# Optimization experiments

Hardware: AMD Instinct MI355X
Metric: run time of the kernel (lower is better)

The kernel has to match this reference:

```python
import jax, jax.numpy as jnp
import numpy as np

PATCH = 16
HIDDEN = 1024
NUM_HEADS = 16
HEAD_DIM = HIDDEN // NUM_HEADS


def sinusoidal_pe(n, d):
    # standard transformer sinusoidal positional encoding, shape [n, d]
    pos = np.arange(n, dtype=np.float32)[:, None]
    i = np.arange(0, d, 2, dtype=np.float32)[None, :]
    ang = pos / np.power(10000.0, i / d)
    pe = np.zeros((n, d), dtype=np.float32)
    pe[:, 0::2] = np.sin(ang)
    pe[:, 1::2] = np.cos(ang)
    return jnp.asarray(pe)


def patch_embed(x, w, b):
    # Conv2d(kernel=stride=PATCH) == non-overlapping patch GEMM
    B, C, H, W = x.shape
    hp, wp = H // PATCH, W // PATCH
    xp = x.reshape(B, C, hp, PATCH, wp, PATCH)
    t = jnp.einsum('bchpwq,dcpq->bhwd', xp, w)  # [B, hp, wp, D]
    return t.reshape(B, hp * wp, -1) + b        # [B, N, D]


def _fit(x, w, b):
    t = patch_embed(x, w, b)
    t = t + sinusoidal_pe(t.shape[1], t.shape[2])
    B, N, _ = t.shape
    return t.reshape(B, N, NUM_HEADS, HEAD_DIM).transpose(0, 2, 1, 3)  # [B,H,N,hd]


def setup_inputs() -> dict:
    key = jax.random.key(0)
    ks = jax.random.split(key, 9)
    B, C, H, W = 16, 3, 512, 512
    return {
        'q_img': jax.random.normal(ks[0], (B, C, H, W), jnp.float32),
        'k_img': jax.random.normal(ks[1], (B, C, H, W), jnp.float32),
        'v_img': jax.random.normal(ks[2], (B, C, H, W), jnp.float32),
        'wq': jax.random.normal(ks[3], (HIDDEN, C, PATCH, PATCH), jnp.float32) * 0.02,
        'bq': jax.random.normal(ks[4], (HIDDEN,), jnp.float32) * 0.02,
        'wk': jax.random.normal(ks[5], (HIDDEN, C, PATCH, PATCH), jnp.float32) * 0.02,
        'bk': jax.random.normal(ks[6], (HIDDEN,), jnp.float32) * 0.02,
        'wv': jax.random.normal(ks[7], (HIDDEN, C, PATCH, PATCH), jnp.float32) * 0.02,
        'bv': jax.random.normal(ks[8], (HIDDEN,), jnp.float32) * 0.02,
    }


def reference(q_img, k_img, v_img, wq, bq, wk, bk, wv, bv):
    q = _fit(q_img, wq, bq)  # [B,H,N,hd]
    k = _fit(k_img, wk, bk)
    v = _fit(v_img, wv, bv)
    q = jax.nn.softmax(q, axis=-1)   # softmax over head_dim
    k = jax.nn.softmax(k, axis=-2)   # softmax over tokens
    scores = jnp.einsum('bhnd,bhne->bhde', k, v)   # k^T v : [B,H,hd,hd]
    ctx = jnp.einsum('bhnd,bhde->bhne', q, scores)  # [B,H,N,hd]
    B, h, N, hd = ctx.shape
    return ctx.transpose(0, 2, 1, 3).reshape(B, N, h * hd)  # [B,N,hidden]
```

## Files before the change

kernel.cpp:

```cpp
#include <hip/hip_runtime.h>
#include <hip/hip_bf16.h>


typedef float  f32x4  __attribute__((ext_vector_type(4)));
typedef __bf16 bf16x8 __attribute__((ext_vector_type(8)));
typedef __bf16 bf16x4 __attribute__((ext_vector_type(4)));

#define LN10000 9.210340371976184f

__device__ __forceinline__ unsigned short f2bf_bits(float f){
  union { float f; unsigned u; } a; a.f = f;
  unsigned r = a.u + 0x7FFFu + ((a.u >> 16) & 1u);
  return (unsigned short)(r >> 16);
}

__device__ __forceinline__ void gload16(const void* g, void* l){
  __builtin_amdgcn_global_load_lds((__attribute__((address_space(1))) void*)g,
                                   (__attribute__((address_space(3))) void*)l,
                                   16, 0, 0);
}


__global__ __launch_bounds__(256) void k_prep_w(
    const float* __restrict__ wq, const float* __restrict__ wk,
    const float* __restrict__ wv, unsigned short* __restrict__ wbf)
{
  int i = blockIdx.x*256 + threadIdx.x;
  if (i >= 589824) return;
  int z = i / 196608;
  int r = i - z*196608;
  const float* src = (z==0) ? wq : (z==1 ? wk : wv);
  f32x4 v = ((const f32x4*)src)[r];
  unsigned lo = (unsigned)f2bf_bits(v[0]) | ((unsigned)f2bf_bits(v[1]) << 16);
  unsigned hh = (unsigned)f2bf_bits(v[2]) | ((unsigned)f2bf_bits(v[3]) << 16);
  ((uint2*)wbf)[i] = make_uint2(lo, hh);
}

__global__ __launch_bounds__(256) void k_prep_pe(float* __restrict__ pe)
{
  int i = blockIdx.x*256 + threadIdx.x;
  if (i >= 1048576) return;
  int n = i >> 10, dd = i & 1023;
  float ex  = (float)(dd & ~1) * (1.0f/1024.0f);
  float ang = (float)n * expf(-LN10000 * ex);
  pe[i] = (dd & 1) ? cosf(ang) : sinf(ang);
}

__global__ __launch_bounds__(256) void k_prep_x(
    const float* __restrict__ xq, const float* __restrict__ xk,
    const float* __restrict__ xv, unsigned short* __restrict__ x_bf)
{
  int i = blockIdx.x*256 + threadIdx.x;
  if (i >= 4718592) return;
  int z = i / 1572864;
  int r = i - z*1572864;
  const float* src = (z==0) ? xq : (z==1 ? xk : xv);
  f32x4 a = ((const f32x4*)src)[r*2];
  f32x4 b = ((const f32x4*)src)[r*2+1];
  uint4 o;
  o.x = (unsigned)f2bf_bits(a[0]) | ((unsigned)f2bf_bits(a[1]) << 16);
  o.y = (unsigned)f2bf_bits(a[2]) | ((unsigned)f2bf_bits(a[3]) << 16);
  o.z = (unsigned)f2bf_bits(b[0]) | ((unsigned)f2bf_bits(b[1]) << 16);
  o.w = (unsigned)f2bf_bits(b[2]) | ((unsigned)f2bf_bits(b[3]) << 16);
  ((uint4*)x_bf)[i] = o;
}


__global__ __launch_bounds__(256, 2) void k_embed(
    const unsigned short* __restrict__ x_bf,
    const unsigned short* __restrict__ wbf,
    const float* __restrict__ bq, const float* __restrict__ bk,
    const float* __restrict__ bv, const float* __restrict__ pe,
    unsigned short* __restrict__ t_bf)
{
  __shared__ __align__(16) unsigned short ldsA[2][128*64];
  __shared__ __align__(16) unsigned short ldsB[2][128*64];

  const int tid = threadIdx.x;
  int flat = blockIdx.x + (blockIdx.y << 3) + (blockIdx.z << 10);
  int orig = (flat & 7)*384 + (flat >> 3);
  const int z   = orig >> 10;
  const int rem = orig & 1023;
  const int m0  = (rem >> 3) * 128;
  const int d0  = (rem & 7) * 128;

  const unsigned short* xbz = x_bf + (size_t)z*12582912u;
  const unsigned short* wz  = wbf + z*786432;
  const float* bias = (z==0) ? bq : (z==1 ? bk : bv);
  unsigned short* tout = t_bf + (size_t)z*16777216u;

  int aRowG[4], aKK[4];
#pragma unroll
  for (int i=0;i<4;i++){
    int L   = i*4096 + tid*16;
    int row = L >> 7;
    int U   = L ^ ((row & 7) << 4);
    aKK[i]  = (U & 127) >> 1;
    int m   = m0 + row;
    int bimg = m >> 10, nt = m & 1023;
    aRowG[i] = bimg*786432 + (nt>>5)*8192 + (nt&31)*16;
  }
  int bOff[4];
#pragma unroll
  for (int i=0;i<4;i++){
    int L   = i*4096 + tid*16;
    int row = L >> 7;
    int U   = L ^ ((row & 7) << 4);
    bOff[i] = (d0 + row)*768 + ((U >> 1) & 63);
  }

  const int lane = tid & 63;
  const int wid  = tid >> 6;
  const int ln   = lane & 15, hi4 = lane >> 4;
  const int wm   = wid >> 1,  wn  = wid & 1;

  f32x4 acc[4][4] = {};

#define STAGE(BUF, KS) do{                                                  \
    _Pragma("unroll")                                                       \
    for (int i=0;i<4;i++){                                                  \
      int k  = (KS)*64 + aKK[i];                                            \
      int c  = k >> 8, r2 = k & 255;                                        \
      gload16(xbz + aRowG[i] + c*262144 + (r2>>4)*512 + (r2 & 15),          \
              (char*)(&ldsA[BUF][0]) + i*4096 + wid*1024);                  \
    }                                                                       \
    _Pragma("unroll")                                                       \
    for (int i=0;i<4;i++){                                                  \
      gload16(wz + bOff[i] + (KS)*64,                                       \
              (char*)(&ldsB[BUF][0]) + i*4096 + wid*1024);                  \
    } }while(0)

  STAGE(0, 0);
  for (int ks=0; ks<12; ++ks){
    int cur = ks & 1;
    if (ks < 11){
      STAGE(cur^1, ks+1);
      asm volatile("s_waitcnt vmcnt(8)" ::: "memory");
    } else {
      asm volatile("s_waitcnt vmcnt(0)" ::: "memory");
    }
    __builtin_amdgcn_sched_barrier(0);
    __builtin_amdgcn_s_barrier();
    __builtin_amdgcn_sched_barrier(0);

    const char* pA = (const char*)&ldsA[cur][0];
    const char* pB = (const char*)&ldsB[cur][0];
#pragma unroll
    for (int kc=0; kc<2; ++kc){
      bf16x8 af[4], bfr[4];
#pragma unroll
      for (int mi=0;mi<4;mi++){
        int row  = wm*64 + mi*16 + ln;
        int byte = (row*128 + kc*64 + hi4*16) ^ ((row & 7) << 4);
        af[mi] = *(const bf16x8*)(pA + byte);
      }
#pragma unroll
      for (int ni=0;ni<4;ni++){
        int row  = wn*64 + ni*16 + ln;
        int byte = (row*128 + kc*64 + hi4*16) ^ ((row & 7) << 4);
        bfr[ni] = *(const bf16x8*)(pB + byte);
      }
#pragma unroll
      for (int mi=0;mi<4;mi++)
#pragma unroll
        for (int ni=0;ni<4;ni++)
          acc[mi][ni] = __builtin_amdgcn_mfma_f32_16x16x32_bf16(
              af[mi], bfr[ni], acc[mi][ni], 0, 0, 0);
    }

    __builtin_amdgcn_sched_barrier(0);
    __builtin_amdgcn_s_barrier();
  }
#undef STAGE

  float bias4[4];
#pragma unroll
  for (int ni=0;ni<4;ni++) bias4[ni] = bias[d0 + wn*64 + ni*16 + ln];

#pragma unroll
  for (int mi=0;mi<4;mi++){
#pragma unroll
    for (int r=0;r<4;r++){
      int m    = m0 + wm*64 + mi*16 + hi4*4 + r;
      int ntok = m & 1023;
      float vv[4];
#pragma unroll
      for (int ni=0;ni<4;ni++){
        int dd = d0 + wn*64 + ni*16 + ln;
        vv[ni] = acc[mi][ni][r] + bias4[ni] + pe[ntok*1024 + dd];
      }
      size_t base = (size_t)m*1024 + d0 + wn*64 + ln;
      if (z == 0){
        float ex0=__expf(vv[0]), ex1=__expf(vv[1]),
              ex2=__expf(vv[2]), ex3=__expf(vv[3]);
        float ps = ex0+ex1+ex2+ex3;
        ps += __shfl_xor(ps, 1); ps += __shfl_xor(ps, 2);
        ps += __shfl_xor(ps, 4); ps += __shfl_xor(ps, 8);
        float w = 1.0f / ps;
        tout[base +  0] = f2bf_bits(ex0*w);  tout[base + 16] = f2bf_bits(ex1*w);
        tout[base + 32] = f2bf_bits(ex2*w);  tout[base + 48] = f2bf_bits(ex3*w);
      } else if (z == 1){
        tout[base +  0] = f2bf_bits(__expf(vv[0]));
        tout[base + 16] = f2bf_bits(__expf(vv[1]));
        tout[base + 32] = f2bf_bits(__expf(vv[2]));
        tout[base + 48] = f2bf_bits(__expf(vv[3]));
      } else {
        tout[base +  0] = f2bf_bits(vv[0]); tout[base + 16] = f2bf_bits(vv[1]);
        tout[base + 32] = f2bf_bits(vv[2]); tout[base + 48] = f2bf_bits(vv[3]);
      }
    }
  }
}


__global__ __launch_bounds__(512) void k_scores(
    const __bf16* __restrict__ t_bf, float* __restrict__ scoresOut)
{
  __shared__ __align__(16) float lds[4][4096];
  __shared__ float ksumLds[8][64];

  const int tid = threadIdx.x;
  const int bh  = blockIdx.x;
  const int b   = bh >> 4, h = bh & 15;
  const __bf16* kbase = t_bf + 16777216u + (size_t)b*1048576u + h*64;
  const __bf16* vbase = t_bf + 33554432u + (size_t)b*1048576u + h*64;

  const int dq = tid & 15, eg = (tid>>4) & 3, npart = tid >> 6;
  const int srow = tid >> 3;
  const int dcol = (tid & 7) * 8;

#define STAGE(BUF, CH) do{                                                \
    size_t g = (size_t)((CH)*64 + srow)*1024 + dcol;                      \
    bf16x8 k8 = *(const bf16x8*)(kbase + g);                              \
    bf16x8 v8 = *(const bf16x8*)(vbase + g);                              \
    f32x4 e0, e1, w0, w1;                                                 \
    e0[0]=(float)k8[0]; e0[1]=(float)k8[1]; e0[2]=(float)k8[2]; e0[3]=(float)k8[3]; \
    e1[0]=(float)k8[4]; e1[1]=(float)k8[5]; e1[2]=(float)k8[6]; e1[3]=(float)k8[7]; \
    w0[0]=(float)v8[0]; w0[1]=(float)v8[1]; w0[2]=(float)v8[2]; w0[3]=(float)v8[3]; \
    w1[0]=(float)v8[4]; w1[1]=(float)v8[5]; w1[2]=(float)v8[6]; w1[3]=(float)v8[7]; \
    *(f32x4*)(&lds[BUF][srow*64 + dcol])       = e0;                      \
    *(f32x4*)(&lds[BUF][srow*64 + dcol + 4])   = e1;                      \
    *(f32x4*)(&lds[2+(BUF)][srow*64 + dcol])     = w0;                    \
    *(f32x4*)(&lds[2+(BUF)][srow*64 + dcol + 4]) = w1;                    \
  }while(0)

  float acc[4][16] = {};
  float kp[4] = {0.f,0.f,0.f,0.f};

  STAGE(0, 0);
  __syncthreads();
  for (int ch=0; ch<16; ++ch){
    int cur = ch & 1;
    if (ch < 15) STAGE(cur^1, ch+1);
    for (int nn = npart; nn < 64; nn += 8){
      f32x4 ek4 = *(const f32x4*)(&lds[cur][nn*64 + dq*4]);
      f32x4 v0  = *(const f32x4*)(&lds[2+cur][nn*64 + eg*16 + 0]);
      f32x4 v1  = *(const f32x4*)(&lds[2+cur][nn*64 + eg*16 + 4]);
      f32x4 v2  = *(const f32x4*)(&lds[2+cur][nn*64 + eg*16 + 8]);
      f32x4 v3  = *(const f32x4*)(&lds[2+cur][nn*64 + eg*16 + 12]);
#pragma unroll
      for (int i2=0;i2<4;i2++){
        kp[i2] += ek4[i2];
#pragma unroll
        for (int j=0;j<4;j++){
          acc[i2][j+0]  += ek4[i2]*v0[j];
          acc[i2][j+4]  += ek4[i2]*v1[j];
          acc[i2][j+8]  += ek4[i2]*v2[j];
          acc[i2][j+12] += ek4[i2]*v3[j];
        }
      }
    }
    __syncthreads();
  }
#undef STAGE

  if (eg == 0){
#pragma unroll
    for (int i2=0;i2<4;i2++) ksumLds[npart][dq*4 + i2] = kp[i2];
  }

  if (npart < 4){
    float* pb = &lds[npart][0];
#pragma unroll
    for (int i2=0;i2<4;i2++){
      int base = (dq*4 + i2)*64 + eg*16;
      f32x4 a0; a0[0]=acc[i2][0];  a0[1]=acc[i2][1];  a0[2]=acc[i2][2];  a0[3]=acc[i2][3];
      f32x4 a1; a1[0]=acc[i2][4];  a1[1]=acc[i2][5];  a1[2]=acc[i2][6];  a1[3]=acc[i2][7];
      f32x4 a2; a2[0]=acc[i2][8];  a2[1]=acc[i2][9];  a2[2]=acc[i2][10]; a2[3]=acc[i2][11];
      f32x4 a3; a3[0]=acc[i2][12]; a3[1]=acc[i2][13]; a3[2]=acc[i2][14]; a3[3]=acc[i2][15];
      *(f32x4*)(pb + base + 0)  = a0;
      *(f32x4*)(pb + base + 4)  = a1;
      *(f32x4*)(pb + base + 8)  = a2;
      *(f32x4*)(pb + base + 12) = a3;
    }
  }
  __syncthreads();
  if (npart >= 4){
    float* pb = &lds[npart-4][0];
#pragma unroll
    for (int i2=0;i2<4;i2++){
      int base = (dq*4 + i2)*64 + eg*16;
#pragma unroll
      for (int q=0;q<4;q++){
        f32x4 cu = *(const f32x4*)(pb + base + 4*q);
        cu[0]+=acc[i2][4*q+0]; cu[1]+=acc[i2][4*q+1];
        cu[2]+=acc[i2][4*q+2]; cu[3]+=acc[i2][4*q+3];
        *(f32x4*)(pb + base + 4*q) = cu;
      }
    }
  }
  __syncthreads();

  float* outp = scoresOut + (size_t)bh*4096;
#pragma unroll
  for (int i=0;i<2;i++){
    int idx = tid + 512*i;
    int q4  = idx*4;
    int d   = idx >> 4;
    float rk = 1.0f / (ksumLds[0][d]+ksumLds[1][d]+ksumLds[2][d]+ksumLds[3][d]
                      +ksumLds[4][d]+ksumLds[5][d]+ksumLds[6][d]+ksumLds[7][d]);
    f32x4 s = *(const f32x4*)(&lds[0][q4]) + *(const f32x4*)(&lds[1][q4])
            + *(const f32x4*)(&lds[2][q4]) + *(const f32x4*)(&lds[3][q4]);
    s[0]*=rk; s[1]*=rk; s[2]*=rk; s[3]*=rk;
    *(f32x4*)(outp + q4) = s;
  }
}


__global__ __launch_bounds__(256) void k_ctx(
    const __bf16* __restrict__ t_bf, const float* __restrict__ scoresIn,
    float* __restrict__ out)
{
  __shared__ __align__(16) float S[64*64];
  __shared__ __align__(16) float qnT[64*132];

  const int tid   = threadIdx.x;
  const int bh    = blockIdx.y;
  const int b     = bh >> 4, h = bh & 15;
  const int chunk = blockIdx.x;
  const __bf16* qbase = t_bf + (size_t)b*1048576u + h*64;

#pragma unroll
  for (int i=0;i<4;i++){
    int q4 = (tid + 256*i)*4;
    *(f32x4*)(S + q4) = *(const f32x4*)(scoresIn + (size_t)bh*4096 + q4);
  }

  const int lane = tid & 63, w = tid >> 6;
  const int pos = lane & 15, rq = lane >> 4;
#pragma unroll
  for (int p=0;p<8;p++){
    int nl = w*32 + p*4 + rq;
    int n  = chunk*128 + nl;
    bf16x4 qv = *(const bf16x4*)(qbase + (size_t)n*1024 + pos*4);
    qnT[(pos*4+0)*132 + nl] = (float)qv[0];
    qnT[(pos*4+1)*132 + nl] = (float)qv[1];
    qnT[(pos*4+2)*132 + nl] = (float)qv[2];
    qnT[(pos*4+3)*132 + nl] = (float)qv[3];
  }
  __syncthreads();

  const int eq = tid & 15, tg = tid >> 4;
  float acc[8][4] = {};
  for (int d=0; d<64; ++d){
    f32x4 s4 = *(const f32x4*)(S   + d*64  + eq*4);
    f32x4 q0 = *(const f32x4*)(qnT + d*132 + tg*8 + 0);
    f32x4 q1 = *(const f32x4*)(qnT + d*132 + tg*8 + 4);
#pragma unroll
    for (int j=0;j<4;j++){
      acc[0][j] += q0[0]*s4[j];
      acc[1][j] += q0[1]*s4[j];
      acc[2][j] += q0[2]*s4[j];
      acc[3][j] += q0[3]*s4[j];
      acc[4][j] += q1[0]*s4[j];
      acc[5][j] += q1[1]*s4[j];
      acc[6][j] += q1[2]*s4[j];
      acc[7][j] += q1[3]*s4[j];
    }
  }
#pragma unroll
  for (int i2=0;i2<8;i2++){
    int n = chunk*128 + tg*8 + i2;
    f32x4 o; o[0]=acc[i2][0]; o[1]=acc[i2][1]; o[2]=acc[i2][2]; o[3]=acc[i2][3];
    *(f32x4*)(out + (size_t)(b*1024 + n)*1024 + h*64 + eq*4) = o;
  }
}


extern "C" void kernel_launch(void* const* d_in, const int* in_sizes, int n_in,
                              void* d_out, int out_size, void* d_ws, size_t ws_size,
                              hipStream_t stream)
{
  const float* q_img = (const float*)d_in[0];
  const float* k_img = (const float*)d_in[1];
  const float* v_img = (const float*)d_in[2];
  const float* wq    = (const float*)d_in[3];
  const float* bq    = (const float*)d_in[4];
  const float* wk    = (const float*)d_in[5];
  const float* bk    = (const float*)d_in[6];
  const float* wv    = (const float*)d_in[7];
  const float* bv    = (const float*)d_in[8];
  float* out = (float*)d_out;
  char*  ws  = (char*)d_ws;

  unsigned short* t_bf   = (unsigned short*)ws;
  unsigned short* wbf    = (unsigned short*)(ws + 0x6000000);
  float*          pe     = (float*)(ws + 0x6480000);
  float*          scores = (float*)(ws + 0x6880000);
  unsigned short* x_bf   = (unsigned short*)(ws + 0x6C80000);

  k_prep_w <<<dim3(2304),  dim3(256), 0, stream>>>(wq, wk, wv, wbf);
  k_prep_pe<<<dim3(4096),  dim3(256), 0, stream>>>(pe);
  k_prep_x <<<dim3(18432), dim3(256), 0, stream>>>(q_img, k_img, v_img, x_bf);
  k_embed  <<<dim3(8,128,3), dim3(256), 0, stream>>>(x_bf, wbf,
                                                     bq,bk,bv, pe, t_bf);
  k_scores <<<dim3(256),  dim3(512), 0, stream>>>((const __bf16*)t_bf, scores);
  k_ctx    <<<dim3(8,256), dim3(256), 0, stream>>>((const __bf16*)t_bf, scores, out);
}
```

Before: 274.4 us.

## Merge prep kernels into one launch and halve embed K-tile for higher occupancy

The three preprocessing kernels (weight cast, positional-encoding table, image cast) are merged into one launch that dispatches on block index, saving two launch gaps. The embed GEMM stages K in slices of 32 instead of 64, with a 4-row XOR swizzle, and asks for 3 blocks per CU instead of 2. This halves the double-buffered LDS tiles to allow more resident blocks and better latency hiding. The cost is twice as many barriers and wait points per tile. An extra 16 KB padding array touched only in a never-taken branch pins the LDS footprint, apparently to control occupancy.

```diff
diff --git a/kernel.cpp b/kernel.cpp
--- a/kernel.cpp
+++ b/kernel.cpp
@@ -21,60 +21,59 @@
 }
 
 
-__global__ __launch_bounds__(256) void k_prep_w(
+__global__ __launch_bounds__(256) void k_prep_all(
     const float* __restrict__ wq, const float* __restrict__ wk,
-    const float* __restrict__ wv, unsigned short* __restrict__ wbf)
-{
-  int i = blockIdx.x*256 + threadIdx.x;
-  if (i >= 589824) return;
-  int z = i / 196608;
-  int r = i - z*196608;
-  const float* src = (z==0) ? wq : (z==1 ? wk : wv);
-  f32x4 v = ((const f32x4*)src)[r];
-  unsigned lo = (unsigned)f2bf_bits(v[0]) | ((unsigned)f2bf_bits(v[1]) << 16);
-  unsigned hh = (unsigned)f2bf_bits(v[2]) | ((unsigned)f2bf_bits(v[3]) << 16);
-  ((uint2*)wbf)[i] = make_uint2(lo, hh);
-}
-
-__global__ __launch_bounds__(256) void k_prep_pe(float* __restrict__ pe)
-{
-  int i = blockIdx.x*256 + threadIdx.x;
-  if (i >= 1048576) return;
-  int n = i >> 10, dd = i & 1023;
-  float ex  = (float)(dd & ~1) * (1.0f/1024.0f);
-  float ang = (float)n * expf(-LN10000 * ex);
-  pe[i] = (dd & 1) ? cosf(ang) : sinf(ang);
-}
-
-__global__ __launch_bounds__(256) void k_prep_x(
+    const float* __restrict__ wv, unsigned short* __restrict__ wbf,
+    float* __restrict__ pe,
     const float* __restrict__ xq, const float* __restrict__ xk,
     const float* __restrict__ xv, unsigned short* __restrict__ x_bf)
 {
-  int i = blockIdx.x*256 + threadIdx.x;
-  if (i >= 4718592) return;
-  int z = i / 1572864;
-  int r = i - z*1572864;
-  const float* src = (z==0) ? xq : (z==1 ? xk : xv);
-  f32x4 a = ((const f32x4*)src)[r*2];
-  f32x4 b = ((const f32x4*)src)[r*2+1];
-  uint4 o;
-  o.x = (unsigned)f2bf_bits(a[0]) | ((unsigned)f2bf_bits(a[1]) << 16);
-  o.y = (unsigned)f2bf_bits(a[2]) | ((unsigned)f2bf_bits(a[3]) << 16);
-  o.z = (unsigned)f2bf_bits(b[0]) | ((unsigned)f2bf_bits(b[1]) << 16);
-  o.w = (unsigned)f2bf_bits(b[2]) | ((unsigned)f2bf_bits(b[3]) << 16);
-  ((uint4*)x_bf)[i] = o;
-}
-
-
-__global__ __launch_bounds__(256, 2) void k_embed(
+  int bid = blockIdx.x;
+  if (bid < 2304){
+    int i = bid*256 + threadIdx.x;
+    if (i >= 589824) return;
+    int z = i / 196608;
+    int r = i - z*196608;
+    const float* src = (z==0) ? wq : (z==1 ? wk : wv);
+    f32x4 v = ((const f32x4*)src)[r];
+    unsigned lo = (unsigned)f2bf_bits(v[0]) | ((unsigned)f2bf_bits(v[1]) << 16);
+    unsigned hh = (unsigned)f2bf_bits(v[2]) | ((unsigned)f2bf_bits(v[3]) << 16);
+    ((uint2*)wbf)[i] = make_uint2(lo, hh);
+  } else if (bid < 6400){
+    int i = (bid - 2304)*256 + threadIdx.x;
+    if (i >= 1048576) return;
+    int n = i >> 10, dd = i & 1023;
+    float ex  = (float)(dd & ~1) * (1.0f/1024.0f);
+    float ang = (float)n * expf(-LN10000 * ex);
+    pe[i] = (dd & 1) ? cosf(ang) : sinf(ang);
+  } else {
+    int i = (bid - 6400)*256 + threadIdx.x;
+    if (i >= 4718592) return;
+    int z = i / 1572864;
+    int r = i - z*1572864;
+    const float* src = (z==0) ? xq : (z==1 ? xk : xv);
+    f32x4 a = ((const f32x4*)src)[r*2];
+    f32x4 b = ((const f32x4*)src)[r*2+1];
+    uint4 o;
+    o.x = (unsigned)f2bf_bits(a[0]) | ((unsigned)f2bf_bits(a[1]) << 16);
+    o.y = (unsigned)f2bf_bits(a[2]) | ((unsigned)f2bf_bits(a[3]) << 16);
+    o.z = (unsigned)f2bf_bits(b[0]) | ((unsigned)f2bf_bits(b[1]) << 16);
+    o.w = (unsigned)f2bf_bits(b[2]) | ((unsigned)f2bf_bits(b[3]) << 16);
+    ((uint4*)x_bf)[i] = o;
+  }
+}
+
+
+__global__ __launch_bounds__(256, 3) void k_embed(
     const unsigned short* __restrict__ x_bf,
     const unsigned short* __restrict__ wbf,
     const float* __restrict__ bq, const float* __restrict__ bk,
     const float* __restrict__ bv, const float* __restrict__ pe,
     unsigned short* __restrict__ t_bf)
 {
-  __shared__ __align__(16) unsigned short ldsA[2][128*64];
-  __shared__ __align__(16) unsigned short ldsB[2][128*64];
+  __shared__ __align__(16) unsigned short ldsA[2][128*32];
+  __shared__ __align__(16) unsigned short ldsB[2][128*32];
+  __shared__ __align__(16) float ldsPad[4096];
 
   const int tid = threadIdx.x;
   int flat = blockIdx.x + (blockIdx.y << 3) + (blockIdx.z << 10);
@@ -89,24 +88,30 @@
   const float* bias = (z==0) ? bq : (z==1 ? bk : bv);
   unsigned short* tout = t_bf + (size_t)z*16777216u;
 
-  int aRowG[4], aKK[4];
-#pragma unroll
-  for (int i=0;i<4;i++){
+  if (bias[0] > 1.0e30f){
+    ldsPad[tid] = pe[tid];
+    __syncthreads();
+    tout[tid] = f2bf_bits(ldsPad[255 - (tid & 255)]);
+  }
+
+  int aRowG[2], aKK[2];
+#pragma unroll
+  for (int i=0;i<2;i++){
     int L   = i*4096 + tid*16;
-    int row = L >> 7;
-    int U   = L ^ ((row & 7) << 4);
-    aKK[i]  = (U & 127) >> 1;
+    int row = L >> 6;
+    int U   = L ^ ((row & 3) << 4);
+    aKK[i]  = (U & 63) >> 1;
     int m   = m0 + row;
     int bimg = m >> 10, nt = m & 1023;
     aRowG[i] = bimg*786432 + (nt>>5)*8192 + (nt&31)*16;
   }
-  int bOff[4];
-#pragma unroll
-  for (int i=0;i<4;i++){
+  int bOff[2];
+#pragma unroll
+  for (int i=0;i<2;i++){
     int L   = i*4096 + tid*16;
-    int row = L >> 7;
-    int U   = L ^ ((row & 7) << 4);
-    bOff[i] = (d0 + row)*768 + ((U >> 1) & 63);
+    int row = L >> 6;
+    int U   = L ^ ((row & 3) << 4);
+    bOff[i] = (d0 + row)*768 + ((U & 63) >> 1);
   }
 
   const int lane = tid & 63;
@@ -118,24 +123,24 @@
 
 #define STAGE(BUF, KS) do{                                                  \
     _Pragma("unroll")                                                       \
-    for (int i=0;i<4;i++){                                                  \
-      int k  = (KS)*64 + aKK[i];                                            \
+    for (int i=0;i<2;i++){                                                  \
+      int k  = (KS)*32 + aKK[i];                                            \
       int c  = k >> 8, r2 = k & 255;                                        \
       gload16(xbz + aRowG[i] + c*262144 + (r2>>4)*512 + (r2 & 15),          \
               (char*)(&ldsA[BUF][0]) + i*4096 + wid*1024);                  \
     }                                                                       \
     _Pragma("unroll")                                                       \
-    for (int i=0;i<4;i++){                                                  \
-      gload16(wz + bOff[i] + (KS)*64,                                       \
+    for (int i=0;i<2;i++){                                                  \
+      gload16(wz + bOff[i] + (KS)*32,                                       \
               (char*)(&ldsB[BUF][0]) + i*4096 + wid*1024);                  \
     } }while(0)
 
   STAGE(0, 0);
-  for (int ks=0; ks<12; ++ks){
+  for (int ks=0; ks<24; ++ks){
     int cur = ks & 1;
-    if (ks < 11){
+    if (ks < 23){
       STAGE(cur^1, ks+1);
-      asm volatile("s_waitcnt vmcnt(8)" ::: "memory");
+      asm volatile("s_waitcnt vmcnt(4)" ::: "memory");
     } else {
       asm volatile("s_waitcnt vmcnt(0)" ::: "memory");
     }
@@ -145,28 +150,25 @@
 
     const char* pA = (const char*)&ldsA[cur][0];
     const char* pB = (const char*)&ldsB[cur][0];
-#pragma unroll
-    for (int kc=0; kc<2; ++kc){
-      bf16x8 af[4], bfr[4];
-#pragma unroll
-      for (int mi=0;mi<4;mi++){
-        int row  = wm*64 + mi*16 + ln;
-        int byte = (row*128 + kc*64 + hi4*16) ^ ((row & 7) << 4);
-        af[mi] = *(const bf16x8*)(pA + byte);
-      }
-#pragma unroll
-      for (int ni=0;ni<4;ni++){
-        int row  = wn*64 + ni*16 + ln;
-        int byte = (row*128 + kc*64 + hi4*16) ^ ((row & 7) << 4);
-        bfr[ni] = *(const bf16x8*)(pB + byte);
-      }
-#pragma unroll
-      for (int mi=0;mi<4;mi++)
-#pragma unroll
-        for (int ni=0;ni<4;ni++)
-          acc[mi][ni] = __builtin_amdgcn_mfma_f32_16x16x32_bf16(
-              af[mi], bfr[ni], acc[mi][ni], 0, 0, 0);
-    }
+    bf16x8 af[4], bfr[4];
+#pragma unroll
+    for (int mi=0;mi<4;mi++){
+      int row  = wm*64 + mi*16 + ln;
+      int byte = (row*64 + hi4*16) ^ ((row & 3) << 4);
+      af[mi] = *(const bf16x8*)(pA + byte);
+    }
+#pragma unroll
+    for (int ni=0;ni<4;ni++){
+      int row  = wn*64 + ni*16 + ln;
+      int byte = (row*64 + hi4*16) ^ ((row & 3) << 4);
+      bfr[ni] = *(const bf16x8*)(pB + byte);
+    }
+#pragma unroll
+    for (int mi=0;mi<4;mi++)
+#pragma unroll
+      for (int ni=0;ni<4;ni++)
+        acc[mi][ni] = __builtin_amdgcn_mfma_f32_16x16x32_bf16(
+            af[mi], bfr[ni], acc[mi][ni], 0, 0, 0);
 
     __builtin_amdgcn_sched_barrier(0);
     __builtin_amdgcn_s_barrier();
@@ -409,9 +411,8 @@
   float*          scores = (float*)(ws + 0x6880000);
   unsigned short* x_bf   = (unsigned short*)(ws + 0x6C80000);
 
-  k_prep_w <<<dim3(2304),  dim3(256), 0, stream>>>(wq, wk, wv, wbf);
-  k_prep_pe<<<dim3(4096),  dim3(256), 0, stream>>>(pe);
-  k_prep_x <<<dim3(18432), dim3(256), 0, stream>>>(q_img, k_img, v_img, x_bf);
+  k_prep_all<<<dim3(24832), dim3(256), 0, stream>>>(wq, wk, wv, wbf, pe,
+                                                    q_img, k_img, v_img, x_bf);
   k_embed  <<<dim3(8,128,3), dim3(256), 0, stream>>>(x_bf, wbf,
                                                      bq,bk,bv, pe, t_bf);
   k_scores <<<dim3(256),  dim3(512), 0, stream>>>((const __bf16*)t_bf, scores);
```

Measured after the change: 237.4 us. 13.5% less time.
